# Performance work log

Hardware: AMD Instinct MI355X
Metric: run time of the kernel (lower is better)

Reference implementation:

```python
import jax, jax.numpy as jnp
import numpy as np

N = 100000
E = 1200000
F_IN, HID, LAT = 16, 128, 64
G = 8  # number of graphs
SG_K = 4


def setup_inputs() -> dict:
    key = jax.random.key(0)
    ks = jax.random.split(key, 20)
    x = jax.random.normal(ks[0], (N, F_IN), dtype=jnp.float32)
    edge_index = jax.random.randint(ks[1], (2, E), 0, N, dtype=jnp.int64)
    batch = jnp.sort(jax.random.randint(ks[2], (N,), 0, G, dtype=jnp.int64))

    def lin(k, fan_in, fan_out):
        s = 1.0 / np.sqrt(fan_in)
        k1, k2 = jax.random.split(k)
        W = jax.random.uniform(k1, (fan_in, fan_out), jnp.float32, -s, s)
        b = jax.random.uniform(k2, (fan_out,), jnp.float32, -s, s)
        return W, b

    W1, b1 = lin(ks[3], F_IN, HID)
    W2, b2 = lin(ks[4], HID, LAT)
    Wg1, bg1 = lin(ks[5], LAT, LAT)
    Wg2, bg2 = lin(ks[6], LAT, LAT)
    Wg3, bg3 = lin(ks[7], LAT, LAT)
    Wsg, bsg = lin(ks[8], LAT, LAT)
    Wf1, bf1 = lin(ks[9], LAT, 32)
    Wf2, bf2 = lin(ks[10], 32, 16)
    Wc, bc = lin(ks[11], 16, 1)
    Wcb, bcb = lin(ks[12], 16, 1)
    return dict(x=x, edge_index=edge_index, batch=batch,
                W1=W1, b1=b1, W2=W2, b2=b2,
                Wg1=Wg1, bg1=bg1, Wg2=Wg2, bg2=bg2, Wg3=Wg3, bg3=bg3,
                Wsg=Wsg, bsg=bsg, Wf1=Wf1, bf1=bf1, Wf2=Wf2, bf2=bf2,
                Wc=Wc, bc=bc, Wcb=Wcb, bcb=bcb)


def reference(x, edge_index, batch,
              W1, b1, W2, b2,
              Wg1, bg1, Wg2, bg2, Wg3, bg3,
              Wsg, bsg, Wf1, bf1, Wf2, bf2,
              Wc, bc, Wcb, bcb):
    n = x.shape[0]
    loops = jnp.arange(n, dtype=edge_index.dtype)
    src = jnp.concatenate([edge_index[0], loops])  # add self-loops (PyG default)
    dst = jnp.concatenate([edge_index[1], loops])
    deg = jax.ops.segment_sum(jnp.ones_like(dst, jnp.float32), dst, num_segments=n)
    dis = jnp.where(deg > 0, jax.lax.rsqrt(jnp.maximum(deg, 1.0)), 0.0)
    norm = dis[src] * dis[dst]  # symmetric GCN normalization

    def prop(h):
        # D^{-1/2} (A+I) D^{-1/2} h  via gather -> scale -> scatter-add
        return jax.ops.segment_sum(h[src] * norm[:, None], dst, num_segments=n)

    def gcn(h, W, b):
        return prop(h @ W) + b

    # encoder
    z = jax.nn.relu(gcn(x, W1, b1))
    z = gcn(z, W2, b2)
    # stacked GCNs
    z = jax.nn.relu(gcn(z, Wg1, bg1))
    z = jax.nn.relu(gcn(z, Wg2, bg2))
    z = jax.nn.relu(gcn(z, Wg3, bg3))
    # SGConv: propagate K times, then linear
    h = z
    for _ in range(SG_K):
        h = prop(h)
    z = h @ Wsg + bsg
    # global max pool per graph
    g = jax.ops.segment_max(z, batch, num_segments=G)
    g = jax.nn.relu(g @ Wf1 + bf1)
    g = jax.nn.relu(g @ Wf2 + bf2)
    cpd_pred = g @ Wc + bc
    comb_logits = g @ Wcb + bcb
    return cpd_pred, comb_logits
```

## Files before the change

kernel.cpp:

```cpp
#include <hip/hip_runtime.h>
#include <hip/hip_bf16.h>
#include <math.h>

#define G_GRAPHS 8

__device__ __forceinline__ unsigned fmap(float f) {
    unsigned b = __float_as_uint(f);
    return (b & 0x80000000u) ? ~b : (b | 0x80000000u);
}
__device__ __forceinline__ float funmap(unsigned u) {
    unsigned b = (u & 0x80000000u) ? (u & 0x7fffffffu) : ~u;
    return __uint_as_float(b);
}

__global__ void k_count(const int* __restrict__ dst, int* __restrict__ deg, int E) {
    int e = blockIdx.x * 256 + threadIdx.x;
    if (e < E) atomicAdd(&deg[dst[e]], 1);
}

__global__ void k_dis(const int* __restrict__ deg, float* __restrict__ dis, int N) {
    int i = blockIdx.x * 256 + threadIdx.x;
    if (i < N) dis[i] = rsqrtf((float)(deg[i] + 1));
}

__global__ void k_scanA(const int* __restrict__ deg, int* __restrict__ rowst,
                        int* __restrict__ bsum, int N) {
    __shared__ int s[256];
    int i = blockIdx.x * 256 + threadIdx.x;
    int v = (i < N) ? deg[i] : 0;
    s[threadIdx.x] = v;
    __syncthreads();
    for (int off = 1; off < 256; off <<= 1) {
        int t = (threadIdx.x >= off) ? s[threadIdx.x - off] : 0;
        __syncthreads();
        s[threadIdx.x] += t;
        __syncthreads();
    }
    if (i < N) rowst[i] = s[threadIdx.x] - v;
    if (threadIdx.x == 255) bsum[blockIdx.x] = s[255];
}

__global__ void k_scanB(int* __restrict__ bsum, int NB) {
    __shared__ int s[512];
    int t = threadIdx.x;
    int v = (t < NB) ? bsum[t] : 0;
    s[t] = v;
    __syncthreads();
    for (int off = 1; off < 512; off <<= 1) {
        int x = (t >= off) ? s[t - off] : 0;
        __syncthreads();
        s[t] += x;
        __syncthreads();
    }
    if (t < NB) bsum[t] = s[t] - v;
}

__global__ void k_scanC(int* __restrict__ rowst, const int* __restrict__ bsum, int N) {
    int i = blockIdx.x * 256 + threadIdx.x;
    if (i < N) rowst[i] += bsum[blockIdx.x];
}

__global__ void k_fill(const int* __restrict__ src, const int* __restrict__ dst,
                       const float* __restrict__ dis, const int* __restrict__ rowst,
                       int* __restrict__ cnt, int2* __restrict__ edge, int E) {
    int e = blockIdx.x * 256 + threadIdx.x;
    if (e >= E) return;
    int d = dst[e], s = src[e];
    int p = rowst[d] + atomicAdd(&cnt[d], 1);
    edge[p] = make_int2(s, __float_as_int(dis[s] * dis[d]));
}

__global__ __launch_bounds__(256) void k_prop16(
        const float* __restrict__ x, float* __restrict__ out,
        const float* __restrict__ dis, const int* __restrict__ rowst,
        const int* __restrict__ deg, const int2* __restrict__ edge, int N) {
    int t = threadIdx.x, lane = t & 63, w = t >> 6;
    int grp = lane >> 2, sub = lane & 3;
    int node = blockIdx.x * 64 + w * 16 + grp;
    if (node >= N) return;
    const float4* x4 = (const float4*)x;
    float d = dis[node];
    float4 sf = x4[node * 4 + sub];
    float sc = d * d;
    float ax = sf.x * sc, ay = sf.y * sc, az = sf.z * sc, aw = sf.w * sc;
    int s = rowst[node], dg = deg[node];
    const int2* ep = edge + s;
    int i = 0;
    for (; i + 1 < dg; i += 2) {
        int2 e0 = ep[i], e1 = ep[i + 1];
        float4 r0 = x4[e0.x * 4 + sub];
        float4 r1 = x4[e1.x * 4 + sub];
        float w0 = __int_as_float(e0.y), w1 = __int_as_float(e1.y);
        ax += w0 * r0.x; ay += w0 * r0.y; az += w0 * r0.z; aw += w0 * r0.w;
        ax += w1 * r1.x; ay += w1 * r1.y; az += w1 * r1.z; aw += w1 * r1.w;
    }
    if (i < dg) {
        int2 e0 = ep[i];
        float4 r0 = x4[e0.x * 4 + sub];
        float w0 = __int_as_float(e0.y);
        ax += w0 * r0.x; ay += w0 * r0.y; az += w0 * r0.z; aw += w0 * r0.w;
    }
    ((float4*)out)[node * 4 + sub] = make_float4(ax, ay, az, aw);
}

__global__ __launch_bounds__(256) void k_dense(
        const float* __restrict__ p0, float* __restrict__ out,
        const float* __restrict__ W1, const float* __restrict__ b1,
        const float* __restrict__ W2, int N) {
    __shared__ float zT[4][128][4];
    int t = threadIdx.x, lane = t & 63, w = t >> 6;
    int base = (blockIdx.x * 4 + w) * 4;
    if (base >= N) return;
    float p = p0[base * 16 + lane];
    float z0a = b1[lane], z1a = z0a;
    float zA[4], zB[4];
    float bA = b1[lane], bB = b1[lane + 64];
    #pragma unroll
    for (int j = 0; j < 4; ++j) { zA[j] = bA; zB[j] = bB; }
    #pragma unroll
    for (int k = 0; k < 16; ++k) {
        float w1a = W1[k * 128 + lane];
        float w1b = W1[k * 128 + lane + 64];
        #pragma unroll
        for (int j = 0; j < 4; ++j) {
            float pk = __shfl(p, j * 16 + k);
            zA[j] += pk * w1a;
            zB[j] += pk * w1b;
        }
    }
    #pragma unroll
    for (int j = 0; j < 4; ++j) {
        zT[w][lane][j]      = fmaxf(zA[j], 0.f);
        zT[w][lane + 64][j] = fmaxf(zB[j], 0.f);
    }
    float acc[4] = {0.f, 0.f, 0.f, 0.f};
    #pragma unroll 4
    for (int k = 0; k < 128; ++k) {
        float wk = W2[k * 64 + lane];
        float4 zk = *(const float4*)&zT[w][k][0];
        acc[0] += zk.x * wk; acc[1] += zk.y * wk;
        acc[2] += zk.z * wk; acc[3] += zk.w * wk;
    }
    #pragma unroll
    for (int j = 0; j < 4; ++j)
        if (base + j < N) out[(base + j) * 64 + lane] = acc[j];
}

__global__ __launch_bounds__(256) void k_prop64(
        const float* __restrict__ in, float* __restrict__ out,
        const float* __restrict__ dis, const int* __restrict__ rowst,
        const int* __restrict__ deg, const int2* __restrict__ edge,
        const float* __restrict__ bias, int relu,
        const float* __restrict__ W, const float* __restrict__ gbias, int N) {
    __shared__ float Wlds[64 * 64];
    __shared__ float zbuf[4][2][64];
    int t = threadIdx.x, lane = t & 63, w = t >> 6;
    int q = lane & 15, g = lane >> 4;
    const float4* in4 = (const float4*)in;
    if (W) {
        for (int i = t; i < 64 * 64 / 4; i += 256)
            ((float4*)Wlds)[i] = ((const float4*)W)[i];
        __syncthreads();
    }
    float4 b4 = make_float4(0.f, 0.f, 0.f, 0.f);
    if (bias) b4 = ((const float4*)bias)[q];
    float gb = (W && gbias) ? gbias[lane] : 0.f;
    int wid = blockIdx.x * 4 + w;
    const int stride = gridDim.x * 4 * 2;
    for (int n0 = wid * 2; n0 < N; n0 += stride) {
        int n1 = n0 + 1;
        bool h1 = n1 < N;
        int s0 = rowst[n0], d0 = deg[n0];
        int s1 = h1 ? rowst[n1] : s0, d1 = h1 ? deg[n1] : 0;
        float di0 = dis[n0];
        float di1 = h1 ? dis[n1] : 0.f;
        const int2* e0 = edge + s0;
        const int2* e1 = edge + s1;
        float4 sf0 = in4[n0 * 16 + q];
        float4 sf1 = h1 ? in4[n1 * 16 + q] : sf0;
        float sc0 = di0 * di0 * 0.25f, sc1 = di1 * di1 * 0.25f;
        float a0x = sf0.x*sc0, a0y = sf0.y*sc0, a0z = sf0.z*sc0, a0w = sf0.w*sc0;
        float a1x = sf1.x*sc1, a1y = sf1.y*sc1, a1z = sf1.z*sc1, a1w = sf1.w*sc1;
        int m = d0 > d1 ? d0 : d1;
        for (int base = 0; base < m; base += 8) {
            int i = base + g, j = base + g + 4;
            int2 m0a = e0[(i < d0) ? i : 0];
            int2 m0b = e0[(j < d0) ? j : 0];
            int2 m1a = e1[(i < d1) ? i : 0];
            int2 m1b = e1[(j < d1) ? j : 0];
            float4 r0a = in4[m0a.x * 16 + q];
            float4 r0b = in4[m0b.x * 16 + q];
            float4 r1a = in4[m1a.x * 16 + q];
            float4 r1b = in4[m1b.x * 16 + q];
            float w0a = (i < d0) ? __int_as_float(m0a.y) : 0.f;
            float w0b = (j < d0) ? __int_as_float(m0b.y) : 0.f;
            float w1a = (i < d1) ? __int_as_float(m1a.y) : 0.f;
            float w1b = (j < d1) ? __int_as_float(m1b.y) : 0.f;
            a0x += w0a*r0a.x; a0y += w0a*r0a.y; a0z += w0a*r0a.z; a0w += w0a*r0a.w;
            a0x += w0b*r0b.x; a0y += w0b*r0b.y; a0z += w0b*r0b.z; a0w += w0b*r0b.w;
            a1x += w1a*r1a.x; a1y += w1a*r1a.y; a1z += w1a*r1a.z; a1w += w1a*r1a.w;
            a1x += w1b*r1b.x; a1y += w1b*r1b.y; a1z += w1b*r1b.z; a1w += w1b*r1b.w;
        }
        a0x += __shfl_xor(a0x,16); a0y += __shfl_xor(a0y,16); a0z += __shfl_xor(a0z,16); a0w += __shfl_xor(a0w,16);
        a0x += __shfl_xor(a0x,32); a0y += __shfl_xor(a0y,32); a0z += __shfl_xor(a0z,32); a0w += __shfl_xor(a0w,32);
        a1x += __shfl_xor(a1x,16); a1y += __shfl_xor(a1y,16); a1z += __shfl_xor(a1z,16); a1w += __shfl_xor(a1w,16);
        a1x += __shfl_xor(a1x,32); a1y += __shfl_xor(a1y,32); a1z += __shfl_xor(a1z,32); a1w += __shfl_xor(a1w,32);
        a0x += b4.x; a0y += b4.y; a0z += b4.z; a0w += b4.w;
        a1x += b4.x; a1y += b4.y; a1z += b4.z; a1w += b4.w;
        if (relu) {
            a0x = fmaxf(a0x,0.f); a0y = fmaxf(a0y,0.f); a0z = fmaxf(a0z,0.f); a0w = fmaxf(a0w,0.f);
            a1x = fmaxf(a1x,0.f); a1y = fmaxf(a1y,0.f); a1z = fmaxf(a1z,0.f); a1w = fmaxf(a1w,0.f);
        }
        if (!W) {
            if (g == 0) {
                ((float4*)out)[n0 * 16 + q] = make_float4(a0x, a0y, a0z, a0w);
                if (h1) ((float4*)out)[n1 * 16 + q] = make_float4(a1x, a1y, a1z, a1w);
            }
        } else {
            if (g == 0) {
                ((float4*)zbuf[w][0])[q] = make_float4(a0x, a0y, a0z, a0w);
                ((float4*)zbuf[w][1])[q] = make_float4(a1x, a1y, a1z, a1w);
            }
            float acc0 = gb, acc1 = gb;
            for (int k = 0; k < 64; ++k) {
                float wk = Wlds[k * 64 + lane];
                acc0 += zbuf[w][0][k] * wk;
                acc1 += zbuf[w][1][k] * wk;
            }
            out[n0 * 64 + lane] = acc0;
            if (h1) out[n1 * 64 + lane] = acc1;
        }
    }
}

__global__ void k_pool_init(unsigned* __restrict__ gmax) {
    gmax[blockIdx.x * 64 + threadIdx.x] = fmap(-INFINITY);
}

__global__ void k_pool(const float* __restrict__ z, const int* __restrict__ batch,
                       unsigned* __restrict__ gmax, int N) {
    int f = threadIdx.x & 63, w = threadIdx.x >> 6;
    int base = (blockIdx.x * 4 + w) * 32;
    if (base >= N) return;
    int end = base + 32; if (end > N) end = N;
    int b0 = batch[base], b1 = batch[end - 1];
    if (b0 == b1) {
        float lmax = -INFINITY;
        for (int n = base; n < end; ++n)
            lmax = fmaxf(lmax, z[n * 64 + f]);
        atomicMax(&gmax[b0 * 64 + f], fmap(lmax));
    } else {
        int curb = b0; float lmax = -INFINITY;
        for (int n = base; n < end; ++n) {
            int b = batch[n];
            if (b != curb) {
                atomicMax(&gmax[curb * 64 + f], fmap(lmax));
                curb = b; lmax = -INFINITY;
            }
            lmax = fmaxf(lmax, z[n * 64 + f]);
        }
        atomicMax(&gmax[curb * 64 + f], fmap(lmax));
    }
}

__global__ void k_head(const unsigned* __restrict__ gmax,
                       const float* __restrict__ Wf1, const float* __restrict__ bf1,
                       const float* __restrict__ Wf2, const float* __restrict__ bf2,
                       const float* __restrict__ Wc, const float* __restrict__ bc,
                       const float* __restrict__ Wcb, const float* __restrict__ bcb,
                       float* __restrict__ out) {
    __shared__ float g[8][64], h1[8][32], h2[8][16];
    int t = threadIdx.x;
    for (int i = t; i < 512; i += 64) g[i >> 6][i & 63] = funmap(gmax[i]);
    __syncthreads();
    for (int i = t; i < 256; i += 64) {
        int r = i >> 5, c = i & 31;
        float a = bf1[c];
        for (int k = 0; k < 64; ++k) a += g[r][k] * Wf1[k * 32 + c];
        h1[r][c] = fmaxf(a, 0.f);
    }
    __syncthreads();
    for (int i = t; i < 128; i += 64) {
        int r = i >> 4, c = i & 15;
        float a = bf2[c];
        for (int k = 0; k < 32; ++k) a += h1[r][k] * Wf2[k * 16 + c];
        h2[r][c] = fmaxf(a, 0.f);
    }
    __syncthreads();
    if (t < 16) {
        int r = t & 7;
        bool comb = t >= 8;
        const float* W = comb ? Wcb : Wc;
        float a = comb ? bcb[0] : bc[0];
        for (int k = 0; k < 16; ++k) a += h2[r][k] * W[k];
        out[(comb ? 8 : 0) + r] = a;
    }
}

extern "C" void kernel_launch(void* const* d_in, const int* in_sizes, int n_in,
                              void* d_out, int out_size, void* d_ws, size_t ws_size,
                              hipStream_t stream) {
    const float* x    = (const float*)d_in[0];
    const int*   ei   = (const int*)d_in[1];
    const int*   batch= (const int*)d_in[2];
    const float* W1   = (const float*)d_in[3];
    const float* b1   = (const float*)d_in[4];
    const float* W2   = (const float*)d_in[5];
    const float* b2   = (const float*)d_in[6];
    const float* Wg1  = (const float*)d_in[7];
    const float* bg1  = (const float*)d_in[8];
    const float* Wg2  = (const float*)d_in[9];
    const float* bg2  = (const float*)d_in[10];
    const float* Wg3  = (const float*)d_in[11];
    const float* bg3  = (const float*)d_in[12];
    const float* Wsg  = (const float*)d_in[13];
    const float* bsg  = (const float*)d_in[14];
    const float* Wf1  = (const float*)d_in[15];
    const float* bf1  = (const float*)d_in[16];
    const float* Wf2  = (const float*)d_in[17];
    const float* bf2  = (const float*)d_in[18];
    const float* Wc   = (const float*)d_in[19];
    const float* bc   = (const float*)d_in[20];
    const float* Wcb  = (const float*)d_in[21];
    const float* bcb  = (const float*)d_in[22];

    const int N = in_sizes[0] / 16;
    const int E = in_sizes[1] / 2;
    const int* esrc = ei;
    const int* edst = ei + E;

    char* ws = (char*)d_ws;
    auto alloc = [&](size_t bytes) -> char* {
        char* p = ws;
        ws += (bytes + 255) & ~(size_t)255;
        return p;
    };
    int*      deg   = (int*)alloc((size_t)N * 4);
    int*      cnt   = (int*)alloc((size_t)N * 4);
    int*      rowst = (int*)alloc((size_t)(N + 1) * 4);
    int*      bsum  = (int*)alloc(4096);
    float*    dis   = (float*)alloc((size_t)N * 4);
    int2*     edge  = (int2*)alloc((size_t)(E + 16) * 8);
    float*    p0    = (float*)alloc((size_t)N * 16 * 4);
    float*    bufA  = (float*)alloc((size_t)N * 64 * 4);
    float*    bufB  = (float*)alloc((size_t)N * 64 * 4);
    unsigned* gmax  = (unsigned*)alloc((size_t)G_GRAPHS * 64 * 4);

    hipMemsetAsync(deg, 0, (size_t)N * 4, stream);
    hipMemsetAsync(cnt, 0, (size_t)N * 4, stream);
    hipMemsetAsync(edge + E, 0, 16 * 8, stream);

    const int EB = (E + 255) / 256;
    const int NB = (N + 255) / 256;
    const int PB = 2048;

    k_count<<<EB, 256, 0, stream>>>(edst, deg, E);
    k_dis<<<NB, 256, 0, stream>>>(deg, dis, N);
    k_scanA<<<NB, 256, 0, stream>>>(deg, rowst, bsum, N);
    k_scanB<<<1, 512, 0, stream>>>(bsum, NB);
    k_scanC<<<NB, 256, 0, stream>>>(rowst, bsum, N);
    k_fill<<<EB, 256, 0, stream>>>(esrc, edst, dis, rowst, cnt, edge, E);

    k_prop16<<<(N + 63) / 64, 256, 0, stream>>>(x, p0, dis, rowst, deg, edge, N);
    k_dense<<<(N + 15) / 16, 256, 0, stream>>>(p0, bufA, W1, b1, W2, N);
    k_prop64<<<PB, 256, 0, stream>>>(bufA, bufB, dis, rowst, deg, edge, b2, 0, Wg1, nullptr, N);
    k_prop64<<<PB, 256, 0, stream>>>(bufB, bufA, dis, rowst, deg, edge, bg1, 1, Wg2, nullptr, N);
    k_prop64<<<PB, 256, 0, stream>>>(bufA, bufB, dis, rowst, deg, edge, bg2, 1, Wg3, nullptr, N);
    k_prop64<<<PB, 256, 0, stream>>>(bufB, bufA, dis, rowst, deg, edge, bg3, 1, nullptr, nullptr, N);
    k_prop64<<<PB, 256, 0, stream>>>(bufA, bufB, dis, rowst, deg, edge, nullptr, 0, nullptr, nullptr, N);
    k_prop64<<<PB, 256, 0, stream>>>(bufB, bufA, dis, rowst, deg, edge, nullptr, 0, nullptr, nullptr, N);
    k_prop64<<<PB, 256, 0, stream>>>(bufA, bufB, dis, rowst, deg, edge, nullptr, 0, nullptr, nullptr, N);
    k_prop64<<<PB, 256, 0, stream>>>(bufB, bufA, dis, rowst, deg, edge, nullptr, 0, Wsg, bsg, N);

    k_pool_init<<<G_GRAPHS, 64, 0, stream>>>(gmax);
    k_pool<<<(N + 127) / 128, 256, 0, stream>>>(bufA, batch, gmax, N);
    k_head<<<1, 64, 0, stream>>>(gmax, Wf1, bf1, Wf2, bf2, Wc, bc, Wcb, bcb, (float*)d_out);
}
```

Baseline: 712.0 us.

## Store node feature buffers in fp16 and widen gather unrolling in propagation kernels

Converts the input features and the intermediate 64-wide node feature buffers to fp16 storage while keeping fp32 accumulation. This halves the bytes moved by the gather-heavy propagation kernels, which are bound by random memory access. The edge loops are also unrolled further, so more gathers are in flight at once. The change costs precision: activations are rounded to half at every layer, and the repeated SGConv propagation could build up error against the reference tolerance.

After: 610.5 us (median of 2 runs). 14.3% less time.

```diff
diff --git a/kernel.cpp b/kernel.cpp
--- a/kernel.cpp
+++ b/kernel.cpp
@@ -1,5 +1,6 @@
 #include <hip/hip_runtime.h>
 #include <hip/hip_bf16.h>
+#include <hip/hip_fp16.h>
 #include <math.h>
 
 #define G_GRAPHS 8
@@ -11,6 +12,20 @@
 __device__ __forceinline__ float funmap(unsigned u) {
     unsigned b = (u & 0x80000000u) ? (u & 0x7fffffffu) : ~u;
     return __uint_as_float(b);
+}
+__device__ __forceinline__ void fma_row(float wv, uint2 r,
+                                        float& ax, float& ay, float& az, float& aw) {
+    float2 f01 = __half22float2(*(__half2*)&r.x);
+    float2 f23 = __half22float2(*(__half2*)&r.y);
+    ax += wv * f01.x; ay += wv * f01.y; az += wv * f23.x; aw += wv * f23.y;
+}
+__device__ __forceinline__ uint2 pack4(float ax, float ay, float az, float aw) {
+    __half2 p01 = __float22half2_rn(make_float2(ax, ay));
+    __half2 p23 = __float22half2_rn(make_float2(az, aw));
+    uint2 r;
+    r.x = *(unsigned*)&p01;
+    r.y = *(unsigned*)&p23;
+    return r;
 }
 
 __global__ void k_count(const int* __restrict__ dst, int* __restrict__ deg, int E) {
@@ -70,41 +85,49 @@
     edge[p] = make_int2(s, __float_as_int(dis[s] * dis[d]));
 }
 
+__global__ void k_x2h(const float* __restrict__ x, __half* __restrict__ xh, int n4) {
+    int i = blockIdx.x * 256 + threadIdx.x;
+    if (i >= n4) return;
+    float4 v = ((const float4*)x)[i];
+    ((uint2*)xh)[i] = pack4(v.x, v.y, v.z, v.w);
+}
+
 __global__ __launch_bounds__(256) void k_prop16(
-        const float* __restrict__ x, float* __restrict__ out,
+        const __half* __restrict__ xh, float* __restrict__ out,
         const float* __restrict__ dis, const int* __restrict__ rowst,
         const int* __restrict__ deg, const int2* __restrict__ edge, int N) {
     int t = threadIdx.x, lane = t & 63, w = t >> 6;
     int grp = lane >> 2, sub = lane & 3;
     int node = blockIdx.x * 64 + w * 16 + grp;
     if (node >= N) return;
-    const float4* x4 = (const float4*)x;
+    const uint2* xr = (const uint2*)xh;
     float d = dis[node];
-    float4 sf = x4[node * 4 + sub];
     float sc = d * d;
-    float ax = sf.x * sc, ay = sf.y * sc, az = sf.z * sc, aw = sf.w * sc;
+    float ax = 0.f, ay = 0.f, az = 0.f, aw = 0.f;
+    fma_row(sc, xr[node * 4 + sub], ax, ay, az, aw);
     int s = rowst[node], dg = deg[node];
     const int2* ep = edge + s;
     int i = 0;
-    for (; i + 1 < dg; i += 2) {
-        int2 e0 = ep[i], e1 = ep[i + 1];
-        float4 r0 = x4[e0.x * 4 + sub];
-        float4 r1 = x4[e1.x * 4 + sub];
-        float w0 = __int_as_float(e0.y), w1 = __int_as_float(e1.y);
-        ax += w0 * r0.x; ay += w0 * r0.y; az += w0 * r0.z; aw += w0 * r0.w;
-        ax += w1 * r1.x; ay += w1 * r1.y; az += w1 * r1.z; aw += w1 * r1.w;
-    }
-    if (i < dg) {
+    for (; i + 3 < dg; i += 4) {
+        int2 e0 = ep[i], e1 = ep[i + 1], e2 = ep[i + 2], e3 = ep[i + 3];
+        uint2 r0 = xr[e0.x * 4 + sub];
+        uint2 r1 = xr[e1.x * 4 + sub];
+        uint2 r2 = xr[e2.x * 4 + sub];
+        uint2 r3 = xr[e3.x * 4 + sub];
+        fma_row(__int_as_float(e0.y), r0, ax, ay, az, aw);
+        fma_row(__int_as_float(e1.y), r1, ax, ay, az, aw);
+        fma_row(__int_as_float(e2.y), r2, ax, ay, az, aw);
+        fma_row(__int_as_float(e3.y), r3, ax, ay, az, aw);
+    }
+    for (; i < dg; ++i) {
         int2 e0 = ep[i];
-        float4 r0 = x4[e0.x * 4 + sub];
-        float w0 = __int_as_float(e0.y);
-        ax += w0 * r0.x; ay += w0 * r0.y; az += w0 * r0.z; aw += w0 * r0.w;
+        fma_row(__int_as_float(e0.y), xr[e0.x * 4 + sub], ax, ay, az, aw);
     }
     ((float4*)out)[node * 4 + sub] = make_float4(ax, ay, az, aw);
 }
 
 __global__ __launch_bounds__(256) void k_dense(
-        const float* __restrict__ p0, float* __restrict__ out,
+        const float* __restrict__ p0, __half* __restrict__ out,
         const float* __restrict__ W1, const float* __restrict__ b1,
         const float* __restrict__ W2, int N) {
     __shared__ float zT[4][128][4];
@@ -112,7 +135,6 @@
     int base = (blockIdx.x * 4 + w) * 4;
     if (base >= N) return;
     float p = p0[base * 16 + lane];
-    float z0a = b1[lane], z1a = z0a;
     float zA[4], zB[4];
     float bA = b1[lane], bB = b1[lane + 64];
     #pragma unroll
@@ -143,11 +165,11 @@
     }
     #pragma unroll
     for (int j = 0; j < 4; ++j)
-        if (base + j < N) out[(base + j) * 64 + lane] = acc[j];
+        if (base + j < N) out[(base + j) * 64 + lane] = __float2half(acc[j]);
 }
 
 __global__ __launch_bounds__(256) void k_prop64(
-        const float* __restrict__ in, float* __restrict__ out,
+        const __half* __restrict__ in, __half* __restrict__ out,
         const float* __restrict__ dis, const int* __restrict__ rowst,
         const int* __restrict__ deg, const int2* __restrict__ edge,
         const float* __restrict__ bias, int relu,
@@ -156,7 +178,7 @@
     __shared__ float zbuf[4][2][64];
     int t = threadIdx.x, lane = t & 63, w = t >> 6;
     int q = lane & 15, g = lane >> 4;
-    const float4* in4 = (const float4*)in;
+    const uint2* inr = (const uint2*)in;
     if (W) {
         for (int i = t; i < 64 * 64 / 4; i += 256)
             ((float4*)Wlds)[i] = ((const float4*)W)[i];
@@ -176,30 +198,46 @@
         float di1 = h1 ? dis[n1] : 0.f;
         const int2* e0 = edge + s0;
         const int2* e1 = edge + s1;
-        float4 sf0 = in4[n0 * 16 + q];
-        float4 sf1 = h1 ? in4[n1 * 16 + q] : sf0;
         float sc0 = di0 * di0 * 0.25f, sc1 = di1 * di1 * 0.25f;
-        float a0x = sf0.x*sc0, a0y = sf0.y*sc0, a0z = sf0.z*sc0, a0w = sf0.w*sc0;
-        float a1x = sf1.x*sc1, a1y = sf1.y*sc1, a1z = sf1.z*sc1, a1w = sf1.w*sc1;
+        float a0x = 0.f, a0y = 0.f, a0z = 0.f, a0w = 0.f;
+        float a1x = 0.f, a1y = 0.f, a1z = 0.f, a1w = 0.f;
+        fma_row(sc0, inr[n0 * 16 + q], a0x, a0y, a0z, a0w);
+        fma_row(sc1, inr[(h1 ? n1 : n0) * 16 + q], a1x, a1y, a1z, a1w);
         int m = d0 > d1 ? d0 : d1;
-        for (int base = 0; base < m; base += 8) {
-            int i = base + g, j = base + g + 4;
-            int2 m0a = e0[(i < d0) ? i : 0];
-            int2 m0b = e0[(j < d0) ? j : 0];
-            int2 m1a = e1[(i < d1) ? i : 0];
-            int2 m1b = e1[(j < d1) ? j : 0];
-            float4 r0a = in4[m0a.x * 16 + q];
-            float4 r0b = in4[m0b.x * 16 + q];
-            float4 r1a = in4[m1a.x * 16 + q];
-            float4 r1b = in4[m1b.x * 16 + q];
-            float w0a = (i < d0) ? __int_as_float(m0a.y) : 0.f;
-            float w0b = (j < d0) ? __int_as_float(m0b.y) : 0.f;
-            float w1a = (i < d1) ? __int_as_float(m1a.y) : 0.f;
-            float w1b = (j < d1) ? __int_as_float(m1b.y) : 0.f;
-            a0x += w0a*r0a.x; a0y += w0a*r0a.y; a0z += w0a*r0a.z; a0w += w0a*r0a.w;
-            a0x += w0b*r0b.x; a0y += w0b*r0b.y; a0z += w0b*r0b.z; a0w += w0b*r0b.w;
-            a1x += w1a*r1a.x; a1y += w1a*r1a.y; a1z += w1a*r1a.z; a1w += w1a*r1a.w;
-            a1x += w1b*r1b.x; a1y += w1b*r1b.y; a1z += w1b*r1b.z; a1w += w1b*r1b.w;
+        for (int base = 0; base < m; base += 16) {
+            int i0 = base + g, i1 = i0 + 4, i2 = i0 + 8, i3 = i0 + 12;
+            int2 ma0 = e0[(i0 < d0) ? i0 : 0];
+            int2 ma1 = e0[(i1 < d0) ? i1 : 0];
+            int2 ma2 = e0[(i2 < d0) ? i2 : 0];
+            int2 ma3 = e0[(i3 < d0) ? i3 : 0];
+            int2 mb0 = e1[(i0 < d1) ? i0 : 0];
+            int2 mb1 = e1[(i1 < d1) ? i1 : 0];
+            int2 mb2 = e1[(i2 < d1) ? i2 : 0];
+            int2 mb3 = e1[(i3 < d1) ? i3 : 0];
+            uint2 ra0 = inr[ma0.x * 16 + q];
+            uint2 ra1 = inr[ma1.x * 16 + q];
+            uint2 ra2 = inr[ma2.x * 16 + q];
+            uint2 ra3 = inr[ma3.x * 16 + q];
+            uint2 rb0 = inr[mb0.x * 16 + q];
+            uint2 rb1 = inr[mb1.x * 16 + q];
+            uint2 rb2 = inr[mb2.x * 16 + q];
+            uint2 rb3 = inr[mb3.x * 16 + q];
+            float wa0 = (i0 < d0) ? __int_as_float(ma0.y) : 0.f;
+            float wa1 = (i1 < d0) ? __int_as_float(ma1.y) : 0.f;
+            float wa2 = (i2 < d0) ? __int_as_float(ma2.y) : 0.f;
+            float wa3 = (i3 < d0) ? __int_as_float(ma3.y) : 0.f;
+            float wb0 = (i0 < d1) ? __int_as_float(mb0.y) : 0.f;
+            float wb1 = (i1 < d1) ? __int_as_float(mb1.y) : 0.f;
+            float wb2 = (i2 < d1) ? __int_as_float(mb2.y) : 0.f;
+            float wb3 = (i3 < d1) ? __int_as_float(mb3.y) : 0.f;
+            fma_row(wa0, ra0, a0x, a0y, a0z, a0w);
+            fma_row(wa1, ra1, a0x, a0y, a0z, a0w);
+            fma_row(wa2, ra2, a0x, a0y, a0z, a0w);
+            fma_row(wa3, ra3, a0x, a0y, a0z, a0w);
+            fma_row(wb0, rb0, a1x, a1y, a1z, a1w);
+            fma_row(wb1, rb1, a1x, a1y, a1z, a1w);
+            fma_row(wb2, rb2, a1x, a1y, a1z, a1w);
+            fma_row(wb3, rb3, a1x, a1y, a1z, a1w);
         }
         a0x += __shfl_xor(a0x,16); a0y += __shfl_xor(a0y,16); a0z += __shfl_xor(a0z,16); a0w += __shfl_xor(a0w,16);
         a0x += __shfl_xor(a0x,32); a0y += __shfl_xor(a0y,32); a0z += __shfl_xor(a0z,32); a0w += __shfl_xor(a0w,32);
@@ -213,8 +251,8 @@
         }
         if (!W) {
             if (g == 0) {
-                ((float4*)out)[n0 * 16 + q] = make_float4(a0x, a0y, a0z, a0w);
-                if (h1) ((float4*)out)[n1 * 16 + q] = make_float4(a1x, a1y, a1z, a1w);
+                ((uint2*)out)[n0 * 16 + q] = pack4(a0x, a0y, a0z, a0w);
+                if (h1) ((uint2*)out)[n1 * 16 + q] = pack4(a1x, a1y, a1z, a1w);
             }
         } else {
             if (g == 0) {
@@ -227,8 +265,8 @@
                 acc0 += zbuf[w][0][k] * wk;
                 acc1 += zbuf[w][1][k] * wk;
             }
-            out[n0 * 64 + lane] = acc0;
-            if (h1) out[n1 * 64 + lane] = acc1;
+            out[n0 * 64 + lane] = __float2half(acc0);
+            if (h1) out[n1 * 64 + lane] = __float2half(acc1);
         }
     }
 }
@@ -237,7 +275,7 @@
     gmax[blockIdx.x * 64 + threadIdx.x] = fmap(-INFINITY);
 }
 
-__global__ void k_pool(const float* __restrict__ z, const int* __restrict__ batch,
+__global__ void k_pool(const __half* __restrict__ z, const int* __restrict__ batch,
                        unsigned* __restrict__ gmax, int N) {
     int f = threadIdx.x & 63, w = threadIdx.x >> 6;
     int base = (blockIdx.x * 4 + w) * 32;
@@ -247,7 +285,7 @@
     if (b0 == b1) {
         float lmax = -INFINITY;
         for (int n = base; n < end; ++n)
-            lmax = fmaxf(lmax, z[n * 64 + f]);
+            lmax = fmaxf(lmax, __half2float(z[n * 64 + f]));
         atomicMax(&gmax[b0 * 64 + f], fmap(lmax));
     } else {
         int curb = b0; float lmax = -INFINITY;
@@ -257,7 +295,7 @@
                 atomicMax(&gmax[curb * 64 + f], fmap(lmax));
                 curb = b; lmax = -INFINITY;
             }
-            lmax = fmaxf(lmax, z[n * 64 + f]);
+            lmax = fmaxf(lmax, __half2float(z[n * 64 + f]));
         }
         atomicMax(&gmax[curb * 64 + f], fmap(lmax));
     }
@@ -341,9 +379,10 @@
     int*      bsum  = (int*)alloc(4096);
     float*    dis   = (float*)alloc((size_t)N * 4);
     int2*     edge  = (int2*)alloc((size_t)(E + 16) * 8);
+    __half*   xh    = (__half*)alloc((size_t)N * 16 * 2);
     float*    p0    = (float*)alloc((size_t)N * 16 * 4);
-    float*    bufA  = (float*)alloc((size_t)N * 64 * 4);
-    float*    bufB  = (float*)alloc((size_t)N * 64 * 4);
+    __half*   bufA  = (__half*)alloc((size_t)N * 64 * 2);
+    __half*   bufB  = (__half*)alloc((size_t)N * 64 * 2);
     unsigned* gmax  = (unsigned*)alloc((size_t)G_GRAPHS * 64 * 4);
 
     hipMemsetAsync(deg, 0, (size_t)N * 4, stream);
@@ -360,8 +399,9 @@
     k_scanB<<<1, 512, 0, stream>>>(bsum, NB);
     k_scanC<<<NB, 256, 0, stream>>>(rowst, bsum, N);
     k_fill<<<EB, 256, 0, stream>>>(esrc, edst, dis, rowst, cnt, edge, E);
-
-    k_prop16<<<(N + 63) / 64, 256, 0, stream>>>(x, p0, dis, rowst, deg, edge, N);
+    k_x2h<<<(N * 4 + 255) / 256, 256, 0, stream>>>(x, xh, N * 4);
+
+    k_prop16<<<(N + 63) / 64, 256, 0, stream>>>(xh, p0, dis, rowst, deg, edge, N);
     k_dense<<<(N + 15) / 16, 256, 0, stream>>>(p0, bufA, W1, b1, W2, N);
     k_prop64<<<PB, 256, 0, stream>>>(bufA, bufB, dis, rowst, deg, edge, b2, 0, Wg1, nullptr, N);
     k_prop64<<<PB, 256, 0, stream>>>(bufB, bufA, dis, rowst, deg, edge, bg1, 1, Wg2, nullptr, N);
```
